# Kernel optimization log

Measured on AMD Instinct MI355X. Metric: run time of the kernel, lower is better.

## Reference

```python
import jax, jax.numpy as jnp
import numpy as np

B, N, D, NB = 64, 64, 2048, 8
W = N - NB + 1  # 57 windows
SCALE = 1.0 / np.sqrt(2048.0)
EPS = 1e-5


def setup_inputs() -> dict:
    key = jax.random.key(0)
    ks = jax.random.split(key, 10)
    p = lambda k, shape: jax.random.normal(k, shape, jnp.float32) * 0.02
    return {
        "fc_feats": jax.random.normal(ks[0], (B, N, D), jnp.float32),
        "nsa_wq": p(ks[1], (D, D)), "nsa_bq": jnp.zeros((D,), jnp.float32),
        "nsa_wk": p(ks[2], (D, D)), "nsa_bk": jnp.zeros((D,), jnp.float32),
        "nsa_wv": p(ks[3], (D, D)), "nsa_bv": jnp.zeros((D,), jnp.float32),
        "ds_w": p(ks[4], (W, N)), "ds_b": jnp.zeros((W,), jnp.float32),
        "ln_g": jnp.ones((D,), jnp.float32), "ln_b": jnp.zeros((D,), jnp.float32),
        "sa_wq": p(ks[5], (D, D)), "sa_bq": jnp.zeros((D,), jnp.float32),
        "sa_wk": p(ks[6], (D, D)), "sa_bk": jnp.zeros((D,), jnp.float32),
        "sa_wv": p(ks[7], (D, D)), "sa_bv": jnp.zeros((D,), jnp.float32),
    }


def reference(fc_feats, nsa_wq, nsa_bq, nsa_wk, nsa_bk, nsa_wv, nsa_bv,
              ds_w, ds_b, ln_g, ln_b,
              sa_wq, sa_bq, sa_wk, sa_bk, sa_wv, sa_bv):
    # --- sliding-window neighboring self-attention (vectorized over windows) ---
    idx = jnp.arange(W)[:, None] + jnp.arange(NB)[None, :]       # [W, NB]
    win = fc_feats[:, idx, :]                                     # [B, W, NB, D]
    q = win @ nsa_wq.T + nsa_bq
    k = win @ nsa_wk.T + nsa_bk
    v = win @ nsa_wv.T + nsa_bv
    dot = jnp.einsum('bwid,bwjd->bwij', q, k) * SCALE            # [B, W, NB, NB]
    attn = jax.nn.softmax(dot, axis=-1)
    # seq_len * mean over queries == sum over queries
    nsa = jnp.einsum('bwij,bwjd->bwd', attn, v)                  # [B, W, D]

    # --- downsample Linear over the image axis ---
    # torch: Linear(N->W) on fc_feats.transpose(-1,-2) then transpose back
    new = jnp.einsum('bnd,wn->bwd', fc_feats, ds_w) + ds_b[:, None]  # [B, W, D]

    # --- layernorm(residual) ---
    h = new + nsa
    mu = h.mean(-1, keepdims=True)
    var = ((h - mu) ** 2).mean(-1, keepdims=True)
    hn = (h - mu) / jnp.sqrt(var + EPS) * ln_g + ln_b            # [B, W, D]

    # --- pooled global self-attention ---
    q2 = hn @ sa_wq.T + sa_bq
    k2 = hn @ sa_wk.T + sa_bk
    v2 = hn @ sa_wv.T + sa_bv
    dot2 = jnp.einsum('bid,bjd->bij', q2, k2) * SCALE            # [B, W, W]
    attn2 = jax.nn.softmax(dot2, axis=-1)
    out = jnp.einsum('bij,bjd->bd', attn2, v2)                   # [B, D] (W * mean == sum)
    return out
```

## Files before the change

kernel.cpp:

```cpp
#include <hip/hip_runtime.h>
#include <cstdint>
#include <cstddef>

#define B_    64
#define N_    64
#define D_    2048
#define NB_   8
#define W_    57
#define QKVLD 6144
#define QKLD  4096
#define SCALE_ 0.022097086912079612f

__device__ __forceinline__ float bf2f(unsigned short u){
  union { unsigned int i; float f; } x; x.i = ((unsigned int)u) << 16; return x.f;
}
__device__ __forceinline__ unsigned short f2bf(float f){
  union { float f; unsigned int i; } x; x.f = f;
  unsigned int r = x.i + 0x7fffu + ((x.i >> 16) & 1u);
  return (unsigned short)(r >> 16);
}

__global__ __launch_bounds__(256) void castA(const float* __restrict__ fc,
                                             const float* __restrict__ wq,
                                             const float* __restrict__ wk,
                                             const float* __restrict__ wv,
                                             unsigned short* __restrict__ fc16,
                                             unsigned short* __restrict__ wcat){
  const int i = blockIdx.x * 256 + threadIdx.x;
  float4 v; ushort4* dst;
  if (i < 2097152) {
    v = ((const float4*)fc)[i];
    dst = (ushort4*)fc16 + i;
  } else {
    const int j = i - 2097152;
    const int sel = j >> 20;
    const float* s = (sel == 0) ? wq : (sel == 1) ? wk : wv;
    v = ((const float4*)s)[j & 1048575];
    dst = (ushort4*)wcat + j;
  }
  ushort4 o; o.x = f2bf(v.x); o.y = f2bf(v.y); o.z = f2bf(v.z); o.w = f2bf(v.w);
  *dst = o;
}

__global__ __launch_bounds__(256) void castB3(const float* __restrict__ a,
                                              const float* __restrict__ b,
                                              const float* __restrict__ c,
                                              unsigned short* __restrict__ wcat2,
                                              unsigned short* __restrict__ swv16){
  const int i = blockIdx.x * 256 + threadIdx.x;
  const int sel = i >> 20;
  const int j = i & 1048575;
  const float* s = (sel == 0) ? a : (sel == 1) ? b : c;
  const float4 v = ((const float4*)s)[j];
  ushort4 o; o.x = f2bf(v.x); o.y = f2bf(v.y); o.z = f2bf(v.z); o.w = f2bf(v.w);
  if (sel < 2) ((ushort4*)wcat2)[i] = o;
  else         ((ushort4*)swv16)[j] = o;
}

__global__ __launch_bounds__(256) void bias_all(
    const float* __restrict__ nq, const float* __restrict__ nk, const float* __restrict__ nv,
    const float* __restrict__ sq, const float* __restrict__ sk,
    float* __restrict__ b1, float* __restrict__ b2){
  const int i = blockIdx.x * 256 + threadIdx.x;
  if (i >= 3 * D_) return;
  const int sel = i >> 11, off = i & 2047;
  b1[i] = (sel == 0) ? nq[off] : (sel == 1) ? nk[off] : nv[off];
  if (sel < 2) b2[i] = (sel == 0) ? sq[off] : sk[off];
}

typedef __attribute__((ext_vector_type(8))) short bfrag8;
typedef __attribute__((ext_vector_type(4))) float facc4;

__global__ __launch_bounds__(256, 3) void gemm_bt(
    const unsigned short* __restrict__ A,
    const unsigned short* __restrict__ Bw,
    const float* __restrict__ bias,
    unsigned short* __restrict__ C,
    int N, int K, int perx)
{
  __shared__ __align__(16) unsigned short lA[128 * 32];
  __shared__ __align__(16) unsigned short lB[128 * 32];
  const int flat = blockIdx.x;
  const int xcd = flat & 7;
  const int idx = flat >> 3;
  const int ct = xcd + 8 * (idx % perx);
  const int rt = idx / perx;
  const int t = threadIdx.x;
  const int lane = t & 63, wid = t >> 6;
  const int wm = wid >> 1, wn = wid & 1;
  const size_t rowBase = (size_t)rt * 128;
  const size_t colBase = (size_t)ct * 128;
  const int sr = lane >> 2, sg = lane & 3;

  const unsigned short* gA0 = A  + (rowBase + (size_t)(wid * 16 + sr)) * K + sg * 8;
  const unsigned short* gB0 = Bw + (colBase + (size_t)(wid * 16 + sr)) * K + sg * 8;
  unsigned short* lA0 = &lA[(wid * 16) * 32];
  unsigned short* lB0 = &lB[(wid * 16) * 32];

  facc4 acc[4][4];
  #pragma unroll
  for (int i = 0; i < 4; i++)
    #pragma unroll
    for (int j = 0; j < 4; j++) acc[i][j] = 0;

  const int fm = lane & 15, quad = lane >> 4;
  const unsigned short* aAddr = &lA[(wm * 64 + fm) * 32 + quad * 8];
  const unsigned short* bAddr = &lB[(wn * 64 + fm) * 32 + quad * 8];

#define STAGE(k0) do { \
    __builtin_amdgcn_global_load_lds((const __attribute__((address_space(1))) void*)(gA0 + (k0)),                 (__attribute__((address_space(3))) void*)(lA0),            16, 0, 0); \
    __builtin_amdgcn_global_load_lds((const __attribute__((address_space(1))) void*)(gA0 + (size_t)64*K + (k0)),  (__attribute__((address_space(3))) void*)(lA0 + 64*32),    16, 0, 0); \
    __builtin_amdgcn_global_load_lds((const __attribute__((address_space(1))) void*)(gB0 + (k0)),                 (__attribute__((address_space(3))) void*)(lB0),            16, 0, 0); \
    __builtin_amdgcn_global_load_lds((const __attribute__((address_space(1))) void*)(gB0 + (size_t)64*K + (k0)),  (__attribute__((address_space(3))) void*)(lB0 + 64*32),    16, 0, 0); \
  } while (0)

  STAGE(0);
  __syncthreads();
  for (int kt = 0;;) {
    bfrag8 af[4], bf[4];
    #pragma unroll
    for (int i = 0; i < 4; i++) {
      af[i] = *(const bfrag8*)(aAddr + i * 16 * 32);
      bf[i] = *(const bfrag8*)(bAddr + i * 16 * 32);
    }
    #pragma unroll
    for (int i = 0; i < 4; i++)
      #pragma unroll
      for (int j = 0; j < 4; j++)
        acc[i][j] = __builtin_amdgcn_mfma_f32_16x16x32_bf16(af[i], bf[j], acc[i][j], 0, 0, 0);
    kt += 32;
    if (kt >= K) break;
    __syncthreads();
    STAGE(kt);
    __syncthreads();
  }
#undef STAGE

  #pragma unroll
  for (int i = 0; i < 4; i++) {
    const size_t r0 = rowBase + wm * 64 + i * 16 + quad * 4;
    #pragma unroll
    for (int j = 0; j < 4; j++) {
      const size_t cc = colBase + wn * 64 + j * 16 + fm;
      const float bv = bias[cc];
      #pragma unroll
      for (int rr = 0; rr < 4; rr++)
        C[(r0 + rr) * (size_t)N + cc] = f2bf(acc[i][j][rr] + bv);
    }
  }
}

__global__ __launch_bounds__(256) void scores_kernel(
    const unsigned short* __restrict__ qkv, int rowsPerBatch, int ld,
    float* __restrict__ Spart)
{
  __shared__ __align__(16) unsigned short lq[64 * 32];
  __shared__ __align__(16) unsigned short lk[64 * 32];
  const int b = blockIdx.x, ks = blockIdx.y;
  const int t = threadIdx.x, lane = t & 63, wid = t >> 6;
  const int sr = lane >> 2, sg = lane & 3;
  const unsigned short* gq = qkv + ((size_t)b * rowsPerBatch + wid * 16 + sr) * ld
                             + ks * 256 + sg * 8;
  const unsigned short* gk = gq + 2048;
  unsigned short* lq0 = &lq[(wid * 16) * 32];
  unsigned short* lk0 = &lk[(wid * 16) * 32];
  const int fm = lane & 15, quad = lane >> 4;
  const unsigned short* aAddr = &lq[(wid * 16 + fm) * 32 + quad * 8];

  facc4 acc[4];
  #pragma unroll
  for (int j = 0; j < 4; j++) acc[j] = 0;

#define STAGE2(k0) do { \
    __builtin_amdgcn_global_load_lds((const __attribute__((address_space(1))) void*)(gq + (k0)), (__attribute__((address_space(3))) void*)(lq0), 16, 0, 0); \
    __builtin_amdgcn_global_load_lds((const __attribute__((address_space(1))) void*)(gk + (k0)), (__attribute__((address_space(3))) void*)(lk0), 16, 0, 0); \
  } while (0)

  STAGE2(0);
  __syncthreads();
  for (int kk = 0;;) {
    const bfrag8 af = *(const bfrag8*)aAddr;
    #pragma unroll
    for (int j = 0; j < 4; j++) {
      const bfrag8 bf = *(const bfrag8*)(&lk[(j * 16 + fm) * 32 + quad * 8]);
      acc[j] = __builtin_amdgcn_mfma_f32_16x16x32_bf16(af, bf, acc[j], 0, 0, 0);
    }
    kk += 32;
    if (kk >= 256) break;
    __syncthreads();
    STAGE2(kk);
    __syncthreads();
  }
#undef STAGE2

  float* sp = Spart + (size_t)(b * 8 + ks) * 4096;
  const int r0 = wid * 16 + quad * 4;
  #pragma unroll
  for (int j = 0; j < 4; j++)
    #pragma unroll
    for (int rr = 0; rr < 4; rr++)
      sp[(r0 + rr) * 64 + j * 16 + fm] = acc[j][rr];
}

__global__ __launch_bounds__(256) void outproj(
    const unsigned short* __restrict__ y16, const unsigned short* __restrict__ swv16,
    float* __restrict__ Opart)
{
  __shared__ __align__(16) unsigned short ly[64 * 32];
  __shared__ __align__(16) unsigned short lv[64 * 32];
  const int dt = blockIdx.x, ks = blockIdx.y;
  const int t = threadIdx.x, lane = t & 63, wid = t >> 6;
  const int sr = lane >> 2, sg = lane & 3;
  const unsigned short* gy = y16  + (size_t)(wid * 16 + sr) * 2048 + ks * 256 + sg * 8;
  const unsigned short* gv = swv16 + (size_t)(dt * 64 + wid * 16 + sr) * 2048 + ks * 256 + sg * 8;
  unsigned short* ly0 = &ly[(wid * 16) * 32];
  unsigned short* lv0 = &lv[(wid * 16) * 32];
  const int fm = lane & 15, quad = lane >> 4;
  const unsigned short* aAddr = &ly[(wid * 16 + fm) * 32 + quad * 8];

  facc4 acc[4];
  #pragma unroll
  for (int j = 0; j < 4; j++) acc[j] = 0;

#define STAGE3(k0) do { \
    __builtin_amdgcn_global_load_lds((const __attribute__((address_space(1))) void*)(gy + (k0)), (__attribute__((address_space(3))) void*)(ly0), 16, 0, 0); \
    __builtin_amdgcn_global_load_lds((const __attribute__((address_space(1))) void*)(gv + (k0)), (__attribute__((address_space(3))) void*)(lv0), 16, 0, 0); \
  } while (0)

  STAGE3(0);
  __syncthreads();
  for (int kk = 0;;) {
    const bfrag8 af = *(const bfrag8*)aAddr;
    #pragma unroll
    for (int j = 0; j < 4; j++) {
      const bfrag8 bf = *(const bfrag8*)(&lv[(j * 16 + fm) * 32 + quad * 8]);
      acc[j] = __builtin_amdgcn_mfma_f32_16x16x32_bf16(af, bf, acc[j], 0, 0, 0);
    }
    kk += 32;
    if (kk >= 256) break;
    __syncthreads();
    STAGE3(kk);
    __syncthreads();
  }
#undef STAGE3

  float* op = Opart + (size_t)ks * 131072 + (size_t)dt * 64;
  const int r0 = wid * 16 + quad * 4;
  #pragma unroll
  for (int j = 0; j < 4; j++)
    #pragma unroll
    for (int rr = 0; rr < 4; rr++)
      op[(size_t)(r0 + rr) * 2048 + j * 16 + fm] = acc[j][rr];
}

__global__ __launch_bounds__(256) void outfin(const float* __restrict__ Opart,
                                              const float* __restrict__ c2buf,
                                              const float* __restrict__ sbv,
                                              float* __restrict__ out){
  const int i = blockIdx.x * 256 + threadIdx.x;
  const int b = i >> 11, d = i & 2047;
  float s = 0.f;
  #pragma unroll
  for (int ks = 0; ks < 8; ks++) s += Opart[(size_t)ks * 131072 + i];
  out[i] = s + c2buf[(size_t)b * 64 + 63] * sbv[d];
}

__global__ __launch_bounds__(512) void nsa_fin(const float* __restrict__ Spart,
                                               float* __restrict__ cbuf){
  __shared__ float Ss[64][65];
  const int b = blockIdx.x, t = threadIdx.x;
  const float* sp = Spart + (size_t)b * 8 * 4096;
  for (int idx = t; idx < 4096; idx += 512) {
    float s = 0.f;
    #pragma unroll
    for (int ks = 0; ks < 8; ks++) s += sp[ks * 4096 + idx];
    Ss[idx >> 6][idx & 63] = s * SCALE_;
  }
  __syncthreads();
  if (t < W_ * 8) {
    const int wi = t >> 3, jp = t & 7;
    float csum = 0.f;
    for (int ip = 0; ip < 8; ip++) {
      const float* row = &Ss[wi + ip][wi];
      float mx = row[0];
      #pragma unroll
      for (int q = 1; q < 8; q++) mx = fmaxf(mx, row[q]);
      float s = 0.f, ej = 0.f;
      #pragma unroll
      for (int q = 0; q < 8; q++) { float e = __expf(row[q] - mx); s += e; if (q == jp) ej = e; }
      csum += ej / s;
    }
    cbuf[((size_t)b * W_ + wi) * 8 + jp] = csum;
  }
}

__global__ __launch_bounds__(512) void sa2_c2(const float* __restrict__ Spart,
                                              float* __restrict__ c2buf){
  __shared__ float Ss[64][65];
  __shared__ float rowm[64], rowsum[64], c2s[64];
  const int b = blockIdx.x, t = threadIdx.x;
  const float* sp = Spart + (size_t)b * 8 * 4096;
  for (int idx = t; idx < 4096; idx += 512) {
    float s = 0.f;
    #pragma unroll
    for (int ks = 0; ks < 8; ks++) s += sp[ks * 4096 + idx];
    Ss[idx >> 6][idx & 63] = s * SCALE_;
  }
  __syncthreads();
  if (t < W_) {
    float mx = -1e30f;
    for (int j = 0; j < W_; j++) mx = fmaxf(mx, Ss[t][j]);
    float s = 0.f;
    for (int j = 0; j < W_; j++) s += __expf(Ss[t][j] - mx);
    rowm[t] = mx; rowsum[t] = 1.f / s;
  }
  __syncthreads();
  if (t < W_) {
    float cs = 0.f;
    for (int i = 0; i < W_; i++) cs += __expf(Ss[i][t] - rowm[i]) * rowsum[i];
    c2s[t] = cs;
    c2buf[(size_t)b * 64 + t] = cs;
  }
  __syncthreads();
  if (t == 0) {
    float s = 0.f;
    for (int j = 0; j < W_; j++) s += c2s[j];
    c2buf[(size_t)b * 64 + 63] = s;
  }
}

__global__ __launch_bounds__(256) void ycomb(const unsigned short* __restrict__ hn,
                                             const float* __restrict__ c2buf,
                                             unsigned short* __restrict__ y16){
  const int b = blockIdx.y;
  const int d = blockIdx.x * 256 + threadIdx.x;
  __shared__ float c2[W_];
  if (threadIdx.x < W_) c2[threadIdx.x] = c2buf[(size_t)b * 64 + threadIdx.x];
  __syncthreads();
  const unsigned short* hrow = hn + (size_t)b * W_ * 2048 + d;
  float a = 0.f;
  for (int j = 0; j < W_; j++) a += c2[j] * bf2f(hrow[(size_t)j * 2048]);
  y16[(size_t)b * 2048 + d] = f2bf(a);
}

__global__ __launch_bounds__(256) void h_kernel(
    const unsigned short* __restrict__ fc16, const float* __restrict__ dsw,
    const float* __restrict__ dsb, const unsigned short* __restrict__ qkv,
    const float* __restrict__ cbuf, float* __restrict__ h)
{
  const int b = blockIdx.y;
  const int d = blockIdx.x * 256 + threadIdx.x;
  __shared__ __align__(16) float dswl[W_ * 64];
  __shared__ float dsbl[W_];
  __shared__ float cl[W_ * 8];
  for (int i = threadIdx.x; i < W_ * 64; i += 256) dswl[i] = dsw[i];
  for (int i = threadIdx.x; i < W_ * 8; i += 256) cl[i] = cbuf[(size_t)b * W_ * 8 + i];
  if (threadIdx.x < W_) dsbl[threadIdx.x] = dsb[threadIdx.x];
  __syncthreads();
  float f[64];
  #pragma unroll
  for (int n = 0; n < 64; n++) f[n] = bf2f(fc16[((size_t)b * 64 + n) * 2048 + d]);
  const unsigned short* vcol = qkv + (size_t)b * 64 * QKVLD + 4096 + d;
  float* hcol = h + (size_t)b * W_ * 2048 + d;
  for (int w = 0; w < W_; w++) {
    float acc = dsbl[w];
    const float4* dw4 = (const float4*)&dswl[w * 64];
    #pragma unroll
    for (int n4 = 0; n4 < 16; n4++) {
      const float4 dv = dw4[n4];
      acc += f[4*n4+0]*dv.x + f[4*n4+1]*dv.y + f[4*n4+2]*dv.z + f[4*n4+3]*dv.w;
    }
    float an = 0.f;
    #pragma unroll
    for (int j = 0; j < 8; j++) an += cl[w * 8 + j] * bf2f(vcol[(size_t)(w + j) * QKVLD]);
    hcol[(size_t)w * 2048] = acc + an;
  }
}

__global__ __launch_bounds__(256) void ln_kernel(
    const float* __restrict__ h, const float* __restrict__ g,
    const float* __restrict__ be, unsigned short* __restrict__ hn)
{
  const int r = blockIdx.x, t = threadIdx.x;
  unsigned short* orow = hn + (size_t)r * 2048;
  if (r >= B_ * W_) {
    for (int i = t; i < 2048; i += 256) orow[i] = 0;
    return;
  }
  const float* row = h + (size_t)r * 2048;
  const float4 v0 = ((const float4*)row)[t];
  const float4 v1 = ((const float4*)row)[t + 256];
  float s  = v0.x + v0.y + v0.z + v0.w + v1.x + v1.y + v1.z + v1.w;
  float s2 = v0.x*v0.x + v0.y*v0.y + v0.z*v0.z + v0.w*v0.w
           + v1.x*v1.x + v1.y*v1.y + v1.z*v1.z + v1.w*v1.w;
  #pragma unroll
  for (int off = 32; off >= 1; off >>= 1) { s += __shfl_down(s, off); s2 += __shfl_down(s2, off); }
  __shared__ float rs[4], rs2[4];
  if ((t & 63) == 0) { rs[t >> 6] = s; rs2[t >> 6] = s2; }
  __syncthreads();
  const float st  = rs[0] + rs[1] + rs[2] + rs[3];
  const float s2t = rs2[0] + rs2[1] + rs2[2] + rs2[3];
  const float mu  = st * (1.f / 2048.f);
  const float var = s2t * (1.f / 2048.f) - mu * mu;
  const float rstd = rsqrtf(var + 1e-5f);
  const float4 g0 = ((const float4*)g)[t],  g1 = ((const float4*)g)[t + 256];
  const float4 b0 = ((const float4*)be)[t], b1 = ((const float4*)be)[t + 256];
  ushort4 o0, o1;
  o0.x = f2bf((v0.x - mu) * rstd * g0.x + b0.x);
  o0.y = f2bf((v0.y - mu) * rstd * g0.y + b0.y);
  o0.z = f2bf((v0.z - mu) * rstd * g0.z + b0.z);
  o0.w = f2bf((v0.w - mu) * rstd * g0.w + b0.w);
  o1.x = f2bf((v1.x - mu) * rstd * g1.x + b1.x);
  o1.y = f2bf((v1.y - mu) * rstd * g1.y + b1.y);
  o1.z = f2bf((v1.z - mu) * rstd * g1.z + b1.z);
  o1.w = f2bf((v1.w - mu) * rstd * g1.w + b1.w);
  ((ushort4*)orow)[t] = o0;
  ((ushort4*)orow)[t + 256] = o1;
}

extern "C" void kernel_launch(void* const* d_in, const int* in_sizes, int n_in,
                              void* d_out, int out_size, void* d_ws, size_t ws_size,
                              hipStream_t stream)
{
  const float* fc  = (const float*)d_in[0];
  const float* nwq = (const float*)d_in[1];
  const float* nbq = (const float*)d_in[2];
  const float* nwk = (const float*)d_in[3];
  const float* nbk = (const float*)d_in[4];
  const float* nwv = (const float*)d_in[5];
  const float* nbv = (const float*)d_in[6];
  const float* dsw = (const float*)d_in[7];
  const float* dsb = (const float*)d_in[8];
  const float* lng = (const float*)d_in[9];
  const float* lnb = (const float*)d_in[10];
  const float* swq = (const float*)d_in[11];
  const float* sbq = (const float*)d_in[12];
  const float* swk = (const float*)d_in[13];
  const float* sbk = (const float*)d_in[14];
  const float* swv = (const float*)d_in[15];
  const float* sbv = (const float*)d_in[16];
  (void)sbk;

  char* ws = (char*)d_ws;
  unsigned short* fc16  = (unsigned short*)(ws + 0);
  unsigned short* wcat  = (unsigned short*)(ws + 16777216);
  float* Spart          = (float*)(ws + 16777216);
  unsigned short* wcat2 = (unsigned short*)(ws + 25165824);
  float* bcat1          = (float*)(ws + 41943040);
  float* bcat2          = (float*)(ws + 41967616);
  unsigned short* qkv   = (unsigned short*)(ws + 41992192);
  float* cbuf           = (float*)(ws + 92323840);
  float* c2buf          = (float*)(ws + 92323840);
  float* hbuf           = (float*)(ws + 92440576);
  unsigned short* swv16 = (unsigned short*)(ws + 92440576);
  unsigned short* y16   = (unsigned short*)(ws + 100829184);
  float* Opart          = (float*)(ws + 101091328);
  unsigned short* hn    = (unsigned short*)(ws + 122324992);

  castA<<<20480, 256, 0, stream>>>(fc, nwq, nwk, nwv, fc16, wcat);
  bias_all<<<24, 256, 0, stream>>>(nbq, nbk, nbv, sbq, sbk, bcat1, bcat2);

  gemm_bt<<<32 * 48, 256, 0, stream>>>(fc16, wcat, bcat1, qkv, 6144, 2048, 6);

  scores_kernel<<<dim3(64, 8), 256, 0, stream>>>(qkv, 64, QKVLD, Spart);
  nsa_fin<<<64, 512, 0, stream>>>(Spart, cbuf);

  h_kernel<<<dim3(8, 64), 256, 0, stream>>>(fc16, dsw, dsb, qkv, cbuf, hbuf);

  ln_kernel<<<3712, 256, 0, stream>>>(hbuf, lng, lnb, hn);

  castB3<<<12288, 256, 0, stream>>>(swq, swk, swv, wcat2, swv16);

  gemm_bt<<<29 * 32, 256, 0, stream>>>(hn, wcat2, bcat2, qkv, 4096, 2048, 4);

  scores_kernel<<<dim3(64, 8), 256, 0, stream>>>(qkv, W_, QKLD, Spart);
  sa2_c2<<<64, 512, 0, stream>>>(Spart, c2buf);

  ycomb<<<dim3(8, 64), 256, 0, stream>>>(hn, c2buf, y16);
  outproj<<<dim3(32, 8), 256, 0, stream>>>(y16, swv16, Opart);
  outfin<<<512, 256, 0, stream>>>(Opart, c2buf, sbv, (float*)d_out);

  (void)in_sizes; (void)n_in; (void)out_size; (void)ws_size;
}
```

Baseline: 512.1 us.

## Fuse residual h computation with layernorm and fold bias setup into cast kernel

Merges the downsample+neighbor-attention residual kernel with the layernorm kernel. Each block now handles 8 windows across the full 2048-wide row, so LN statistics are reduced in-block and the fp32 h buffer round trip is gone. The bias-concatenation kernel is folded into the cast kernel's tail blocks, saving one launch. The fused kernel runs only 520 blocks and keeps a large per-thread accumulator (64 floats), which risks register pressure, and it rereads fc16 rows per window group.

```diff
diff --git a/kernel.cpp b/kernel.cpp
--- a/kernel.cpp
+++ b/kernel.cpp
@@ -24,9 +24,23 @@
                                              const float* __restrict__ wq,
                                              const float* __restrict__ wk,
                                              const float* __restrict__ wv,
+                                             const float* __restrict__ nq,
+                                             const float* __restrict__ nk,
+                                             const float* __restrict__ nv,
+                                             const float* __restrict__ sq,
+                                             const float* __restrict__ sk,
                                              unsigned short* __restrict__ fc16,
-                                             unsigned short* __restrict__ wcat){
+                                             unsigned short* __restrict__ wcat,
+                                             float* __restrict__ b1,
+                                             float* __restrict__ b2){
   const int i = blockIdx.x * 256 + threadIdx.x;
+  if (i >= 5242880) {
+    const int k = i - 5242880;
+    const int sel = k >> 11, off = k & 2047;
+    b1[k] = (sel == 0) ? nq[off] : (sel == 1) ? nk[off] : nv[off];
+    if (sel < 2) b2[k] = (sel == 0) ? sq[off] : sk[off];
+    return;
+  }
   float4 v; ushort4* dst;
   if (i < 2097152) {
     v = ((const float4*)fc)[i];
@@ -55,17 +69,6 @@
   ushort4 o; o.x = f2bf(v.x); o.y = f2bf(v.y); o.z = f2bf(v.z); o.w = f2bf(v.w);
   if (sel < 2) ((ushort4*)wcat2)[i] = o;
   else         ((ushort4*)swv16)[j] = o;
-}
-
-__global__ __launch_bounds__(256) void bias_all(
-    const float* __restrict__ nq, const float* __restrict__ nk, const float* __restrict__ nv,
-    const float* __restrict__ sq, const float* __restrict__ sk,
-    float* __restrict__ b1, float* __restrict__ b2){
-  const int i = blockIdx.x * 256 + threadIdx.x;
-  if (i >= 3 * D_) return;
-  const int sel = i >> 11, off = i & 2047;
-  b1[i] = (sel == 0) ? nq[off] : (sel == 1) ? nk[off] : nv[off];
-  if (sel < 2) b2[i] = (sel == 0) ? sq[off] : sk[off];
 }
 
 typedef __attribute__((ext_vector_type(8))) short bfrag8;
@@ -343,79 +346,104 @@
   y16[(size_t)b * 2048 + d] = f2bf(a);
 }
 
-__global__ __launch_bounds__(256) void h_kernel(
+typedef __attribute__((ext_vector_type(8))) unsigned short us8;
+__global__ __launch_bounds__(256) void hln_kernel(
     const unsigned short* __restrict__ fc16, const float* __restrict__ dsw,
     const float* __restrict__ dsb, const unsigned short* __restrict__ qkv,
-    const float* __restrict__ cbuf, float* __restrict__ h)
-{
-  const int b = blockIdx.y;
-  const int d = blockIdx.x * 256 + threadIdx.x;
-  __shared__ __align__(16) float dswl[W_ * 64];
-  __shared__ float dsbl[W_];
-  __shared__ float cl[W_ * 8];
-  for (int i = threadIdx.x; i < W_ * 64; i += 256) dswl[i] = dsw[i];
-  for (int i = threadIdx.x; i < W_ * 8; i += 256) cl[i] = cbuf[(size_t)b * W_ * 8 + i];
-  if (threadIdx.x < W_) dsbl[threadIdx.x] = dsb[threadIdx.x];
-  __syncthreads();
-  float f[64];
-  #pragma unroll
-  for (int n = 0; n < 64; n++) f[n] = bf2f(fc16[((size_t)b * 64 + n) * 2048 + d]);
-  const unsigned short* vcol = qkv + (size_t)b * 64 * QKVLD + 4096 + d;
-  float* hcol = h + (size_t)b * W_ * 2048 + d;
-  for (int w = 0; w < W_; w++) {
-    float acc = dsbl[w];
-    const float4* dw4 = (const float4*)&dswl[w * 64];
-    #pragma unroll
-    for (int n4 = 0; n4 < 16; n4++) {
-      const float4 dv = dw4[n4];
-      acc += f[4*n4+0]*dv.x + f[4*n4+1]*dv.y + f[4*n4+2]*dv.z + f[4*n4+3]*dv.w;
-    }
-    float an = 0.f;
-    #pragma unroll
-    for (int j = 0; j < 8; j++) an += cl[w * 8 + j] * bf2f(vcol[(size_t)(w + j) * QKVLD]);
-    hcol[(size_t)w * 2048] = acc + an;
-  }
-}
-
-__global__ __launch_bounds__(256) void ln_kernel(
-    const float* __restrict__ h, const float* __restrict__ g,
+    const float* __restrict__ cbuf, const float* __restrict__ g,
     const float* __restrict__ be, unsigned short* __restrict__ hn)
 {
-  const int r = blockIdx.x, t = threadIdx.x;
-  unsigned short* orow = hn + (size_t)r * 2048;
-  if (r >= B_ * W_) {
-    for (int i = t; i < 2048; i += 256) orow[i] = 0;
+  const int flat = blockIdx.x;
+  const int t = threadIdx.x;
+  if (flat >= 512) {
+    const int p = flat - 512;
+    unsigned short* orow = hn + (size_t)(3648 + p * 8) * 2048;
+    for (int i = t; i < 8 * 2048; i += 256) orow[i] = 0;
     return;
   }
-  const float* row = h + (size_t)r * 2048;
-  const float4 v0 = ((const float4*)row)[t];
-  const float4 v1 = ((const float4*)row)[t + 256];
-  float s  = v0.x + v0.y + v0.z + v0.w + v1.x + v1.y + v1.z + v1.w;
-  float s2 = v0.x*v0.x + v0.y*v0.y + v0.z*v0.z + v0.w*v0.w
-           + v1.x*v1.x + v1.y*v1.y + v1.z*v1.z + v1.w*v1.w;
-  #pragma unroll
-  for (int off = 32; off >= 1; off >>= 1) { s += __shfl_down(s, off); s2 += __shfl_down(s2, off); }
-  __shared__ float rs[4], rs2[4];
-  if ((t & 63) == 0) { rs[t >> 6] = s; rs2[t >> 6] = s2; }
-  __syncthreads();
-  const float st  = rs[0] + rs[1] + rs[2] + rs[3];
-  const float s2t = rs2[0] + rs2[1] + rs2[2] + rs2[3];
-  const float mu  = st * (1.f / 2048.f);
-  const float var = s2t * (1.f / 2048.f) - mu * mu;
-  const float rstd = rsqrtf(var + 1e-5f);
-  const float4 g0 = ((const float4*)g)[t],  g1 = ((const float4*)g)[t + 256];
-  const float4 b0 = ((const float4*)be)[t], b1 = ((const float4*)be)[t + 256];
-  ushort4 o0, o1;
-  o0.x = f2bf((v0.x - mu) * rstd * g0.x + b0.x);
-  o0.y = f2bf((v0.y - mu) * rstd * g0.y + b0.y);
-  o0.z = f2bf((v0.z - mu) * rstd * g0.z + b0.z);
-  o0.w = f2bf((v0.w - mu) * rstd * g0.w + b0.w);
-  o1.x = f2bf((v1.x - mu) * rstd * g1.x + b1.x);
-  o1.y = f2bf((v1.y - mu) * rstd * g1.y + b1.y);
-  o1.z = f2bf((v1.z - mu) * rstd * g1.z + b1.z);
-  o1.w = f2bf((v1.w - mu) * rstd * g1.w + b1.w);
-  ((ushort4*)orow)[t] = o0;
-  ((ushort4*)orow)[t + 256] = o1;
+  const int wg = flat >> 6, b = flat & 63;
+  const int w0 = wg * 8;
+  const int nw = (wg == 7) ? 1 : 8;
+  __shared__ float dswl[8 * 64];
+  __shared__ float cl[8 * 8];
+  __shared__ float dsbl[8];
+  __shared__ float red[4][8][2];
+  for (int i = t; i < nw * 64; i += 256) dswl[i] = dsw[(w0 + (i >> 6)) * 64 + (i & 63)];
+  for (int i = t; i < nw * 8; i += 256) cl[i] = cbuf[((size_t)b * W_ + w0 + (i >> 3)) * 8 + (i & 7)];
+  if (t < nw) dsbl[t] = dsb[w0 + t];
+  __syncthreads();
+
+  const int d0 = t * 8;
+  float acc[8][8];
+  #pragma unroll
+  for (int w = 0; w < 8; w++)
+    #pragma unroll
+    for (int p = 0; p < 8; p++) acc[w][p] = 0.f;
+
+  for (int n = 0; n < 64; n++) {
+    const us8 fv8 = *(const us8*)(fc16 + ((size_t)b * 64 + n) * 2048 + d0);
+    float fv[8];
+    #pragma unroll
+    for (int p = 0; p < 8; p++) fv[p] = bf2f(fv8[p]);
+    for (int w = 0; w < nw; w++) {
+      const float dv = dswl[w * 64 + n];
+      #pragma unroll
+      for (int p = 0; p < 8; p++) acc[w][p] += fv[p] * dv;
+    }
+  }
+  for (int r = 0; r < nw + 7; r++) {
+    const us8 vv8 = *(const us8*)(qkv + ((size_t)b * 64 + w0 + r) * QKVLD + 4096 + d0);
+    float vv[8];
+    #pragma unroll
+    for (int p = 0; p < 8; p++) vv[p] = bf2f(vv8[p]);
+    #pragma unroll
+    for (int j = 0; j < 8; j++) {
+      const int w = r - j;
+      if (w >= 0 && w < nw) {
+        const float cv = cl[w * 8 + j];
+        #pragma unroll
+        for (int p = 0; p < 8; p++) acc[w][p] += cv * vv[p];
+      }
+    }
+  }
+  float s1[8], s2v[8];
+  for (int w = 0; w < nw; w++) {
+    const float bb = dsbl[w];
+    float a1 = 0.f, a2 = 0.f;
+    #pragma unroll
+    for (int p = 0; p < 8; p++) {
+      acc[w][p] += bb;
+      a1 += acc[w][p];
+      a2 += acc[w][p] * acc[w][p];
+    }
+    s1[w] = a1; s2v[w] = a2;
+  }
+  const int wv = t >> 6, lane = t & 63;
+  for (int w = 0; w < nw; w++) {
+    #pragma unroll
+    for (int off = 32; off >= 1; off >>= 1) {
+      s1[w]  += __shfl_down(s1[w], off);
+      s2v[w] += __shfl_down(s2v[w], off);
+    }
+    if (lane == 0) { red[wv][w][0] = s1[w]; red[wv][w][1] = s2v[w]; }
+  }
+  __syncthreads();
+  const float4 g0 = *(const float4*)(g + d0),  g1 = *(const float4*)(g + d0 + 4);
+  const float4 e0 = *(const float4*)(be + d0), e1 = *(const float4*)(be + d0 + 4);
+  const float gp[8] = {g0.x,g0.y,g0.z,g0.w,g1.x,g1.y,g1.z,g1.w};
+  const float ep[8] = {e0.x,e0.y,e0.z,e0.w,e1.x,e1.y,e1.z,e1.w};
+  for (int w = 0; w < nw; w++) {
+    const float st  = red[0][w][0] + red[1][w][0] + red[2][w][0] + red[3][w][0];
+    const float st2 = red[0][w][1] + red[1][w][1] + red[2][w][1] + red[3][w][1];
+    const float mu  = st * (1.f / 2048.f);
+    const float var = st2 * (1.f / 2048.f) - mu * mu;
+    const float rstd = rsqrtf(var + 1e-5f);
+    us8 o;
+    #pragma unroll
+    for (int p = 0; p < 8; p++)
+      o[p] = f2bf((acc[w][p] - mu) * rstd * gp[p] + ep[p]);
+    *(us8*)(hn + (size_t)(b * W_ + w0 + w) * 2048 + d0) = o;
+  }
 }
 
 extern "C" void kernel_launch(void* const* d_in, const int* in_sizes, int n_in,
@@ -451,23 +479,20 @@
   unsigned short* qkv   = (unsigned short*)(ws + 41992192);
   float* cbuf           = (float*)(ws + 92323840);
   float* c2buf          = (float*)(ws + 92323840);
-  float* hbuf           = (float*)(ws + 92440576);
   unsigned short* swv16 = (unsigned short*)(ws + 92440576);
   unsigned short* y16   = (unsigned short*)(ws + 100829184);
   float* Opart          = (float*)(ws + 101091328);
   unsigned short* hn    = (unsigned short*)(ws + 122324992);
 
-  castA<<<20480, 256, 0, stream>>>(fc, nwq, nwk, nwv, fc16, wcat);
-  bias_all<<<24, 256, 0, stream>>>(nbq, nbk, nbv, sbq, sbk, bcat1, bcat2);
+  castA<<<20504, 256, 0, stream>>>(fc, nwq, nwk, nwv, nbq, nbk, nbv, sbq, sbk,
+                                   fc16, wcat, bcat1, bcat2);
 
   gemm_bt<<<32 * 48, 256, 0, stream>>>(fc16, wcat, bcat1, qkv, 6144, 2048, 6);
 
   scores_kernel<<<dim3(64, 8), 256, 0, stream>>>(qkv, 64, QKVLD, Spart);
   nsa_fin<<<64, 512, 0, stream>>>(Spart, cbuf);
 
-  h_kernel<<<dim3(8, 64), 256, 0, stream>>>(fc16, dsw, dsb, qkv, cbuf, hbuf);
-
-  ln_kernel<<<3712, 256, 0, stream>>>(hbuf, lng, lnb, hn);
+  hln_kernel<<<520, 256, 0, stream>>>(fc16, dsw, dsb, qkv, cbuf, lng, lnb, hn);
 
   castB3<<<12288, 256, 0, stream>>>(swq, swk, swv, wcat2, swv16);
 
```

New measurement: 946.5 us. 1.85x slower.
